# Kernel tuning notes

Measured on AMD Instinct MI355X. Metric: run time of the kernel, lower is better.

Reference implementation:

```python
import jax, jax.numpy as jnp
import numpy as np

B, T, C = 4, 2048, 1024
H = 16
D = C // H  # 64


def setup_inputs() -> dict:
    key = jax.random.key(0)
    ks = jax.random.split(key, 3)
    scale = 1.0 / np.sqrt(C)
    return {
        "x": jax.random.normal(ks[0], (B, T, C), dtype=jnp.float32),
        "W_attn": jax.random.normal(ks[1], (C, 3 * C), dtype=jnp.float32) * scale,
        "b_attn": jnp.zeros((3 * C,), dtype=jnp.float32),
        "W_proj": jax.random.normal(ks[2], (C, C), dtype=jnp.float32) * scale,
        "b_proj": jnp.zeros((C,), dtype=jnp.float32),
    }


def reference(x, W_attn, b_attn, W_proj, b_proj):
    b, t, c = x.shape
    qkv = x @ W_attn + b_attn                      # [B,T,3C]
    q, k, v = jnp.split(qkv, 3, axis=-1)           # each [B,T,C]
    to_heads = lambda z: z.reshape(b, t, H, D).transpose(0, 2, 1, 3)  # [B,H,T,D]
    q, k, v = to_heads(q), to_heads(k), to_heads(v)
    scores = jnp.einsum("bhtd,bhsd->bhts", q, k) / jnp.sqrt(jnp.float32(D))
    causal = jnp.tril(jnp.ones((t, t), dtype=bool))  # [T,T]
    scores = jnp.where(causal[None, None], scores, jnp.finfo(scores.dtype).min)
    attn = jax.nn.softmax(scores, axis=-1)           # [B,H,T,T]
    out = jnp.einsum("bhts,bhsd->bhtd", attn, v)     # [B,H,T,D]
    out = out.transpose(0, 2, 1, 3).reshape(b, t, c)
    return out @ W_proj + b_proj
```

## Files before the change

kernel.cpp:

```cpp
#include <hip/hip_runtime.h>
#include <hip/hip_bf16.h>

typedef __bf16 bf16_t;
typedef __attribute__((ext_vector_type(8))) __bf16 bf16x8;
typedef __attribute__((ext_vector_type(4))) float f32x4;
typedef __attribute__((ext_vector_type(4))) unsigned short u16x4;

#define B_DIM 4
#define T_DIM 2048
#define C_DIM 1024
#define H_DIM 16
#define D_DIM 64
#define M_TOK (B_DIM * T_DIM)
#define N_QKV (3 * C_DIM)
#define NT    (T_DIM / 64)
#define KSTR  72
#define CSC   0.18033688011112042f

__device__ __forceinline__ void gload_lds16(const bf16_t* g, bf16_t* l) {
  __builtin_amdgcn_global_load_lds((const __attribute__((address_space(1))) void*)(g),
                                   (__attribute__((address_space(3))) void*)(l), 16, 0, 0);
}

#define CVT_BLOCKS 8192
#define TRA_BLOCKS 3072
#define TRP_BLOCKS 1024
__global__ void preprocess(const float* __restrict__ x, bf16_t* __restrict__ xb,
                           const float* __restrict__ W_attn, bf16_t* __restrict__ Wat,
                           const float* __restrict__ W_proj, bf16_t* __restrict__ Wpt) {
  __shared__ float tile[32][33];
  const int bid = blockIdx.x;
  const int tid = threadIdx.x;
  if (bid < CVT_BLOCKS) {
    int i = bid * 256 + tid;
    float4 v = ((const float4*)x)[i];
    struct alignas(8) bv4 { bf16_t a, b, c, d; };
    bv4 o = {(bf16_t)v.x, (bf16_t)v.y, (bf16_t)v.z, (bf16_t)v.w};
    ((bv4*)xb)[i] = o;
    return;
  }
  const float* in; bf16_t* outp; int N, local;
  if (bid < CVT_BLOCKS + TRA_BLOCKS) {
    local = bid - CVT_BLOCKS; in = W_attn; outp = Wat; N = N_QKV;
  } else {
    local = bid - CVT_BLOCKS - TRA_BLOCKS; in = W_proj; outp = Wpt; N = C_DIM;
  }
  const int K = C_DIM;
  const int nbx = N / 32;
  const int bx = (local % nbx) * 32, by = (local / nbx) * 32;
  const int tx = tid & 31, ty = tid >> 5;
#pragma unroll
  for (int i = 0; i < 32; i += 8)
    tile[ty + i][tx] = in[(size_t)(by + ty + i) * N + bx + tx];
  __syncthreads();
#pragma unroll
  for (int i = 0; i < 32; i += 8)
    outp[(size_t)(bx + ty + i) * K + by + tx] = (bf16_t)tile[tx][ty + i];
}

#define BM 128
#define BN 128
#define BKG 64

template <typename OutT>
__global__ __launch_bounds__(256, 4)
void gemm_bt_bias(const bf16_t* __restrict__ A, const bf16_t* __restrict__ Bt,
                  const float* __restrict__ bias, OutT* __restrict__ C,
                  int M, int N, int K) {
  __shared__ alignas(16) bf16_t As[BM * BKG];
  __shared__ alignas(16) bf16_t Bs[BN * BKG];
  const int tid = threadIdx.x;
  const int lane = tid & 63;
  const int wave = tid >> 6;
  const int wr = (wave >> 1) * 64, wc = (wave & 1) * 64;
  const int quad = lane >> 4, l16 = lane & 15;
  const int row0 = blockIdx.x * BM, col0 = blockIdx.y * BN;

  const int srow = wave * 8 + (lane >> 3);
  const int scol = ((lane & 7) ^ (lane >> 3)) * 8;
  const bf16_t* Ag = A + (size_t)(row0 + srow) * K + scol;
  const bf16_t* Bg = Bt + (size_t)(col0 + srow) * K + scol;

  f32x4 acc[4][4];
#pragma unroll
  for (int i = 0; i < 4; ++i)
#pragma unroll
    for (int j = 0; j < 4; ++j)
      acc[i][j] = (f32x4){0.f, 0.f, 0.f, 0.f};

  for (int k0 = 0; k0 < K; k0 += BKG) {
    __syncthreads();
#pragma unroll
    for (int c = 0; c < 4; ++c)
      gload_lds16(Ag + k0 + (size_t)(c * 32) * K, &As[(c * 32 + wave * 8) * BKG]);
#pragma unroll
    for (int c = 0; c < 4; ++c)
      gload_lds16(Bg + k0 + (size_t)(c * 32) * K, &Bs[(c * 32 + wave * 8) * BKG]);
    __syncthreads();
#pragma unroll
    for (int kk = 0; kk < 2; ++kk) {
      const int sl = (kk * 4 + quad) ^ (l16 & 7);
      bf16x8 af[4], bfr[4];
#pragma unroll
      for (int i = 0; i < 4; ++i)
        af[i] = *(const bf16x8*)&As[(wr + i * 16 + l16) * BKG + sl * 8];
#pragma unroll
      for (int j = 0; j < 4; ++j)
        bfr[j] = *(const bf16x8*)&Bs[(wc + j * 16 + l16) * BKG + sl * 8];
#pragma unroll
      for (int i = 0; i < 4; ++i)
#pragma unroll
        for (int j = 0; j < 4; ++j)
          acc[i][j] = __builtin_amdgcn_mfma_f32_16x16x32_bf16(af[i], bfr[j], acc[i][j], 0, 0, 0);
    }
  }

#pragma unroll
  for (int i = 0; i < 4; ++i)
#pragma unroll
    for (int j = 0; j < 4; ++j) {
      int col = col0 + wc + j * 16 + l16;
      float bv = bias[col];
#pragma unroll
      for (int r = 0; r < 4; ++r) {
        int row = row0 + wr + i * 16 + quad * 4 + r;
        C[(size_t)row * N + col] = (OutT)(acc[i][j][r] + bv);
      }
    }
}

__device__ __forceinline__ float exp_row_sum(f32x4 sv[4], bool diag, bf16_t* PsW,
                                             int l16, int quad, int wave) {
  if (diag) {
    const int qr = wave * 16 + l16;
#pragma unroll
    for (int ct = 0; ct < 4; ++ct)
#pragma unroll
      for (int r = 0; r < 4; ++r)
        if (ct * 16 + quad * 4 + r > qr) sv[ct][r] = -INFINITY;
  }
  float rsum = 0.f;
#pragma unroll
  for (int ct = 0; ct < 4; ++ct) {
    u16x4 pk;
#pragma unroll
    for (int r = 0; r < 4; ++r) {
      float p = __builtin_amdgcn_exp2f(sv[ct][r] * CSC);
      rsum += p;
      pk[r] = __builtin_bit_cast(unsigned short, (bf16_t)p);
    }
    *(u16x4*)&PsW[l16 * KSTR + ct * 16 + quad * 4] = pk;
  }
  rsum += __shfl_xor(rsum, 16);
  rsum += __shfl_xor(rsum, 32);
  return rsum;
}

__global__ __launch_bounds__(256, 4)
void attn_fwd(const bf16_t* __restrict__ qkv, bf16_t* __restrict__ out) {
  __shared__ alignas(16) bf16_t Ks[64 * KSTR];
  __shared__ alignas(16) bf16_t Vt[64 * KSTR];
  __shared__ alignas(16) bf16_t Ps[4 * 16 * KSTR];

  const int tid = threadIdx.x;
  const int lane = tid & 63;
  const int wave = tid >> 6;
  const int quad = lane >> 4, l16 = lane & 15;
  const int qlo = blockIdx.x;
  const int qhi = NT - 1 - qlo;
  const int h = blockIdx.y, b = blockIdx.z;
  const size_t tokBase = (size_t)b * T_DIM;

  const bf16_t* qpl = qkv + (tokBase + qlo * 64 + wave * 16 + l16) * N_QKV + h * D_DIM;
  const bf16_t* qph = qkv + (tokBase + qhi * 64 + wave * 16 + l16) * N_QKV + h * D_DIM;
  bf16x8 ql0 = *(const bf16x8*)(qpl + quad * 8);
  bf16x8 ql1 = *(const bf16x8*)(qpl + 32 + quad * 8);
  bf16x8 qh0 = *(const bf16x8*)(qph + quad * 8);
  bf16x8 qh1 = *(const bf16x8*)(qph + 32 + quad * 8);

  f32x4 ol[4], oh[4];
#pragma unroll
  for (int dt = 0; dt < 4; ++dt) {
    ol[dt] = (f32x4){0.f, 0.f, 0.f, 0.f};
    oh[dt] = (f32x4){0.f, 0.f, 0.f, 0.f};
  }
  float ll = 0.f, lh = 0.f;

  const int tx = tid & 15, ty = tid >> 4;
  const int vswz = ((tx >> 2) & 3) * 8;
  bf16_t* PsW = &Ps[wave * 16 * KSTR];
  const f32x4 zero4 = (f32x4){0.f, 0.f, 0.f, 0.f};

  u16x4 kreg[4], vreg[4];
  const bf16_t* kb0 = qkv + (tokBase + ty * 4) * N_QKV + h * D_DIM + C_DIM + tx * 4;
#pragma unroll
  for (int r = 0; r < 4; ++r) kreg[r] = *(const u16x4*)(kb0 + (size_t)r * N_QKV);
#pragma unroll
  for (int r = 0; r < 4; ++r) vreg[r] = *(const u16x4*)(kb0 + (size_t)r * N_QKV + C_DIM);

  for (int t = 0; t <= qhi; ++t) {
    const bool lo = (t <= qlo);
    __syncthreads();
#pragma unroll
    for (int r = 0; r < 4; ++r)
      *(u16x4*)&Ks[(ty * 4 + r) * KSTR + tx * 4] = kreg[r];
#pragma unroll
    for (int i = 0; i < 4; ++i) {
      u16x4 p = (u16x4){vreg[0][i], vreg[1][i], vreg[2][i], vreg[3][i]};
      *(u16x4*)&Vt[(tx * 4 + i) * KSTR + ((ty * 4) ^ vswz)] = p;
    }
    __syncthreads();
    if (t < qhi) {
      const bf16_t* kb = qkv + (tokBase + (t + 1) * 64 + ty * 4) * N_QKV + h * D_DIM + C_DIM + tx * 4;
#pragma unroll
      for (int r = 0; r < 4; ++r) kreg[r] = *(const u16x4*)(kb + (size_t)r * N_QKV);
#pragma unroll
      for (int r = 0; r < 4; ++r) vreg[r] = *(const u16x4*)(kb + (size_t)r * N_QKV + C_DIM);
    }

    f32x4 svl[4], svh[4];
#pragma unroll
    for (int ct = 0; ct < 4; ++ct) {
      bf16x8 kf0 = *(const bf16x8*)&Ks[(ct * 16 + l16) * KSTR + quad * 8];
      bf16x8 kf1 = *(const bf16x8*)&Ks[(ct * 16 + l16) * KSTR + 32 + quad * 8];
      if (lo) {
        svl[ct] = __builtin_amdgcn_mfma_f32_16x16x32_bf16(kf0, ql0, zero4, 0, 0, 0);
        svl[ct] = __builtin_amdgcn_mfma_f32_16x16x32_bf16(kf1, ql1, svl[ct], 0, 0, 0);
      }
      svh[ct] = __builtin_amdgcn_mfma_f32_16x16x32_bf16(kf0, qh0, zero4, 0, 0, 0);
      svh[ct] = __builtin_amdgcn_mfma_f32_16x16x32_bf16(kf1, qh1, svh[ct], 0, 0, 0);
    }

    bf16x8 pl0, pl1, ph0, ph1;
    if (lo) {
      ll += exp_row_sum(svl, t == qlo, PsW, l16, quad, wave);
      pl0 = *(const bf16x8*)&PsW[l16 * KSTR + quad * 8];
      pl1 = *(const bf16x8*)&PsW[l16 * KSTR + 32 + quad * 8];
    }
    lh += exp_row_sum(svh, t == qhi, PsW, l16, quad, wave);
    ph0 = *(const bf16x8*)&PsW[l16 * KSTR + quad * 8];
    ph1 = *(const bf16x8*)&PsW[l16 * KSTR + 32 + quad * 8];

#pragma unroll
    for (int dt = 0; dt < 4; ++dt) {
      const int vcol = (quad * 8) ^ ((dt & 3) * 8);
      bf16x8 vf0 = *(const bf16x8*)&Vt[(dt * 16 + l16) * KSTR + vcol];
      bf16x8 vf1 = *(const bf16x8*)&Vt[(dt * 16 + l16) * KSTR + 32 + vcol];
      if (lo) {
        ol[dt] = __builtin_amdgcn_mfma_f32_16x16x32_bf16(vf0, pl0, ol[dt], 0, 0, 0);
        ol[dt] = __builtin_amdgcn_mfma_f32_16x16x32_bf16(vf1, pl1, ol[dt], 0, 0, 0);
      }
      oh[dt] = __builtin_amdgcn_mfma_f32_16x16x32_bf16(vf0, ph0, oh[dt], 0, 0, 0);
      oh[dt] = __builtin_amdgcn_mfma_f32_16x16x32_bf16(vf1, ph1, oh[dt], 0, 0, 0);
    }
  }

  struct alignas(8) bh4 { bf16_t a, b, c, d; };
  {
    float rl = 1.0f / ll;
    bf16_t* op = out + (tokBase + qlo * 64 + wave * 16 + l16) * C_DIM + h * D_DIM;
#pragma unroll
    for (int dt = 0; dt < 4; ++dt) {
      bh4 v = {(bf16_t)(ol[dt][0] * rl), (bf16_t)(ol[dt][1] * rl),
               (bf16_t)(ol[dt][2] * rl), (bf16_t)(ol[dt][3] * rl)};
      *(bh4*)(op + dt * 16 + quad * 4) = v;
    }
  }
  {
    float rl = 1.0f / lh;
    bf16_t* op = out + (tokBase + qhi * 64 + wave * 16 + l16) * C_DIM + h * D_DIM;
#pragma unroll
    for (int dt = 0; dt < 4; ++dt) {
      bh4 v = {(bf16_t)(oh[dt][0] * rl), (bf16_t)(oh[dt][1] * rl),
               (bf16_t)(oh[dt][2] * rl), (bf16_t)(oh[dt][3] * rl)};
      *(bh4*)(op + dt * 16 + quad * 4) = v;
    }
  }
}

extern "C" void kernel_launch(void* const* d_in, const int* in_sizes, int n_in,
                              void* d_out, int out_size, void* d_ws, size_t ws_size,
                              hipStream_t stream) {
  const float* x      = (const float*)d_in[0];
  const float* W_attn = (const float*)d_in[1];
  const float* b_attn = (const float*)d_in[2];
  const float* W_proj = (const float*)d_in[3];
  const float* b_proj = (const float*)d_in[4];
  float* out = (float*)d_out;

  char* ws = (char*)d_ws;
  bf16_t* xb   = (bf16_t*)ws;  ws += (size_t)M_TOK * C_DIM * 2;
  bf16_t* Wat  = (bf16_t*)ws;  ws += (size_t)N_QKV * C_DIM * 2;
  bf16_t* Wpt  = (bf16_t*)ws;  ws += (size_t)C_DIM * C_DIM * 2;
  bf16_t* qkv  = (bf16_t*)ws;  ws += (size_t)M_TOK * N_QKV * 2;
  bf16_t* attn = (bf16_t*)ws;  ws += (size_t)M_TOK * C_DIM * 2;

  preprocess<<<CVT_BLOCKS + TRA_BLOCKS + TRP_BLOCKS, 256, 0, stream>>>(
      x, xb, W_attn, Wat, W_proj, Wpt);

  gemm_bt_bias<bf16_t><<<dim3(M_TOK / BM, N_QKV / BN), 256, 0, stream>>>(
      xb, Wat, b_attn, qkv, M_TOK, N_QKV, C_DIM);

  attn_fwd<<<dim3(NT / 2, H_DIM, B_DIM), 256, 0, stream>>>(qkv, attn);

  gemm_bt_bias<float><<<dim3(M_TOK / BM, C_DIM / BN), 256, 0, stream>>>(
      attn, Wpt, b_proj, out, M_TOK, C_DIM, C_DIM);
}
```

Before: 256.6 us.

## Keep attention probabilities in registers and use one query tile per block

The attention kernel no longer writes exp'd probabilities to a per-wave LDS buffer and reads them back. It packs them directly into the bf16x8 MFMA operand, and the V tile is stored in LDS with a permuted column layout so the register layout matches the MFMA B operand. The paired lo/hi query-tile scheme is replaced by one query tile per block with a rotated tile index spread across heads and batches, doubling the grid and raising occupancy to 6 blocks. This removes LDS traffic and per-block register pressure, at the cost of uneven per-block work that relies on the scheduler to balance.

Measured after the change: 262.7 us. 1.02x slower.

```diff
diff --git a/kernel.cpp b/kernel.cpp
--- a/kernel.cpp
+++ b/kernel.cpp
@@ -5,6 +5,7 @@
 typedef __attribute__((ext_vector_type(8))) __bf16 bf16x8;
 typedef __attribute__((ext_vector_type(4))) float f32x4;
 typedef __attribute__((ext_vector_type(4))) unsigned short u16x4;
+typedef __attribute__((ext_vector_type(4))) unsigned int u32x4;
 
 #define B_DIM 4
 #define T_DIM 2048
@@ -129,66 +130,31 @@
     }
 }
 
-__device__ __forceinline__ float exp_row_sum(f32x4 sv[4], bool diag, bf16_t* PsW,
-                                             int l16, int quad, int wave) {
-  if (diag) {
-    const int qr = wave * 16 + l16;
-#pragma unroll
-    for (int ct = 0; ct < 4; ++ct)
-#pragma unroll
-      for (int r = 0; r < 4; ++r)
-        if (ct * 16 + quad * 4 + r > qr) sv[ct][r] = -INFINITY;
-  }
-  float rsum = 0.f;
-#pragma unroll
-  for (int ct = 0; ct < 4; ++ct) {
-    u16x4 pk;
-#pragma unroll
-    for (int r = 0; r < 4; ++r) {
-      float p = __builtin_amdgcn_exp2f(sv[ct][r] * CSC);
-      rsum += p;
-      pk[r] = __builtin_bit_cast(unsigned short, (bf16_t)p);
-    }
-    *(u16x4*)&PsW[l16 * KSTR + ct * 16 + quad * 4] = pk;
-  }
-  rsum += __shfl_xor(rsum, 16);
-  rsum += __shfl_xor(rsum, 32);
-  return rsum;
-}
-
-__global__ __launch_bounds__(256, 4)
+__global__ __launch_bounds__(256, 6)
 void attn_fwd(const bf16_t* __restrict__ qkv, bf16_t* __restrict__ out) {
   __shared__ alignas(16) bf16_t Ks[64 * KSTR];
   __shared__ alignas(16) bf16_t Vt[64 * KSTR];
-  __shared__ alignas(16) bf16_t Ps[4 * 16 * KSTR];
 
   const int tid = threadIdx.x;
   const int lane = tid & 63;
   const int wave = tid >> 6;
   const int quad = lane >> 4, l16 = lane & 15;
-  const int qlo = blockIdx.x;
-  const int qhi = NT - 1 - qlo;
   const int h = blockIdx.y, b = blockIdx.z;
+  const int q = (int)((blockIdx.x + h + 2 * b) & 31);
   const size_t tokBase = (size_t)b * T_DIM;
 
-  const bf16_t* qpl = qkv + (tokBase + qlo * 64 + wave * 16 + l16) * N_QKV + h * D_DIM;
-  const bf16_t* qph = qkv + (tokBase + qhi * 64 + wave * 16 + l16) * N_QKV + h * D_DIM;
-  bf16x8 ql0 = *(const bf16x8*)(qpl + quad * 8);
-  bf16x8 ql1 = *(const bf16x8*)(qpl + 32 + quad * 8);
-  bf16x8 qh0 = *(const bf16x8*)(qph + quad * 8);
-  bf16x8 qh1 = *(const bf16x8*)(qph + 32 + quad * 8);
-
-  f32x4 ol[4], oh[4];
-#pragma unroll
-  for (int dt = 0; dt < 4; ++dt) {
-    ol[dt] = (f32x4){0.f, 0.f, 0.f, 0.f};
-    oh[dt] = (f32x4){0.f, 0.f, 0.f, 0.f};
-  }
-  float ll = 0.f, lh = 0.f;
+  const bf16_t* qp = qkv + (tokBase + q * 64 + wave * 16 + l16) * N_QKV + h * D_DIM;
+  bf16x8 q0 = *(const bf16x8*)(qp + quad * 8);
+  bf16x8 q1 = *(const bf16x8*)(qp + 32 + quad * 8);
+
+  f32x4 o[4];
+#pragma unroll
+  for (int dt = 0; dt < 4; ++dt) o[dt] = (f32x4){0.f, 0.f, 0.f, 0.f};
+  float lsum = 0.f;
 
   const int tx = tid & 15, ty = tid >> 4;
   const int vswz = ((tx >> 2) & 3) * 8;
-  bf16_t* PsW = &Ps[wave * 16 * KSTR];
+  const int vcol = (8 * (ty & 3) + 4 * ((ty >> 2) & 1) + 32 * (ty >> 3)) ^ vswz;
   const f32x4 zero4 = (f32x4){0.f, 0.f, 0.f, 0.f};
 
   u16x4 kreg[4], vreg[4];
@@ -198,8 +164,7 @@
 #pragma unroll
   for (int r = 0; r < 4; ++r) vreg[r] = *(const u16x4*)(kb0 + (size_t)r * N_QKV + C_DIM);
 
-  for (int t = 0; t <= qhi; ++t) {
-    const bool lo = (t <= qlo);
+  for (int t = 0; t <= q; ++t) {
     __syncthreads();
 #pragma unroll
     for (int r = 0; r < 4; ++r)
@@ -207,10 +172,10 @@
 #pragma unroll
     for (int i = 0; i < 4; ++i) {
       u16x4 p = (u16x4){vreg[0][i], vreg[1][i], vreg[2][i], vreg[3][i]};
-      *(u16x4*)&Vt[(tx * 4 + i) * KSTR + ((ty * 4) ^ vswz)] = p;
-    }
-    __syncthreads();
-    if (t < qhi) {
+      *(u16x4*)&Vt[(tx * 4 + i) * KSTR + vcol] = p;
+    }
+    __syncthreads();
+    if (t < q) {
       const bf16_t* kb = qkv + (tokBase + (t + 1) * 64 + ty * 4) * N_QKV + h * D_DIM + C_DIM + tx * 4;
 #pragma unroll
       for (int r = 0; r < 4; ++r) kreg[r] = *(const u16x4*)(kb + (size_t)r * N_QKV);
@@ -218,61 +183,65 @@
       for (int r = 0; r < 4; ++r) vreg[r] = *(const u16x4*)(kb + (size_t)r * N_QKV + C_DIM);
     }
 
-    f32x4 svl[4], svh[4];
+    f32x4 sv[4];
 #pragma unroll
     for (int ct = 0; ct < 4; ++ct) {
       bf16x8 kf0 = *(const bf16x8*)&Ks[(ct * 16 + l16) * KSTR + quad * 8];
       bf16x8 kf1 = *(const bf16x8*)&Ks[(ct * 16 + l16) * KSTR + 32 + quad * 8];
-      if (lo) {
-        svl[ct] = __builtin_amdgcn_mfma_f32_16x16x32_bf16(kf0, ql0, zero4, 0, 0, 0);
-        svl[ct] = __builtin_amdgcn_mfma_f32_16x16x32_bf16(kf1, ql1, svl[ct], 0, 0, 0);
-      }
-      svh[ct] = __builtin_amdgcn_mfma_f32_16x16x32_bf16(kf0, qh0, zero4, 0, 0, 0);
-      svh[ct] = __builtin_amdgcn_mfma_f32_16x16x32_bf16(kf1, qh1, svh[ct], 0, 0, 0);
-    }
-
-    bf16x8 pl0, pl1, ph0, ph1;
-    if (lo) {
-      ll += exp_row_sum(svl, t == qlo, PsW, l16, quad, wave);
-      pl0 = *(const bf16x8*)&PsW[l16 * KSTR + quad * 8];
-      pl1 = *(const bf16x8*)&PsW[l16 * KSTR + 32 + quad * 8];
-    }
-    lh += exp_row_sum(svh, t == qhi, PsW, l16, quad, wave);
-    ph0 = *(const bf16x8*)&PsW[l16 * KSTR + quad * 8];
-    ph1 = *(const bf16x8*)&PsW[l16 * KSTR + 32 + quad * 8];
+      sv[ct] = __builtin_amdgcn_mfma_f32_16x16x32_bf16(kf0, q0, zero4, 0, 0, 0);
+      sv[ct] = __builtin_amdgcn_mfma_f32_16x16x32_bf16(kf1, q1, sv[ct], 0, 0, 0);
+    }
+    if (t == q) {
+      const int qr = wave * 16 + l16;
+#pragma unroll
+      for (int ct = 0; ct < 4; ++ct)
+#pragma unroll
+        for (int r = 0; r < 4; ++r)
+          if (ct * 16 + quad * 4 + r > qr) sv[ct][r] = -INFINITY;
+    }
+
+    float rsum = 0.f;
+    unsigned int lw[8];
+    struct alignas(4) bpair { bf16_t lo, hi; };
+#pragma unroll
+    for (int ct = 0; ct < 4; ++ct) {
+      float e0 = __builtin_amdgcn_exp2f(sv[ct][0] * CSC);
+      float e1 = __builtin_amdgcn_exp2f(sv[ct][1] * CSC);
+      float e2 = __builtin_amdgcn_exp2f(sv[ct][2] * CSC);
+      float e3 = __builtin_amdgcn_exp2f(sv[ct][3] * CSC);
+      rsum += (e0 + e1) + (e2 + e3);
+      bpair w0 = {(bf16_t)e0, (bf16_t)e1};
+      bpair w1 = {(bf16_t)e2, (bf16_t)e3};
+      lw[ct * 2 + 0] = __builtin_bit_cast(unsigned int, w0);
+      lw[ct * 2 + 1] = __builtin_bit_cast(unsigned int, w1);
+    }
+    rsum += __shfl_xor(rsum, 16);
+    rsum += __shfl_xor(rsum, 32);
+    lsum += rsum;
+
+    u32x4 pw0 = (u32x4){lw[0], lw[1], lw[2], lw[3]};
+    u32x4 pw1 = (u32x4){lw[4], lw[5], lw[6], lw[7]};
+    bf16x8 p0 = __builtin_bit_cast(bf16x8, pw0);
+    bf16x8 p1 = __builtin_bit_cast(bf16x8, pw1);
 
 #pragma unroll
     for (int dt = 0; dt < 4; ++dt) {
-      const int vcol = (quad * 8) ^ ((dt & 3) * 8);
-      bf16x8 vf0 = *(const bf16x8*)&Vt[(dt * 16 + l16) * KSTR + vcol];
-      bf16x8 vf1 = *(const bf16x8*)&Vt[(dt * 16 + l16) * KSTR + 32 + vcol];
-      if (lo) {
-        ol[dt] = __builtin_amdgcn_mfma_f32_16x16x32_bf16(vf0, pl0, ol[dt], 0, 0, 0);
-        ol[dt] = __builtin_amdgcn_mfma_f32_16x16x32_bf16(vf1, pl1, ol[dt], 0, 0, 0);
-      }
-      oh[dt] = __builtin_amdgcn_mfma_f32_16x16x32_bf16(vf0, ph0, oh[dt], 0, 0, 0);
-      oh[dt] = __builtin_amdgcn_mfma_f32_16x16x32_bf16(vf1, ph1, oh[dt], 0, 0, 0);
+      const int vc = (quad * 8) ^ (dt * 8);
+      bf16x8 vf0 = *(const bf16x8*)&Vt[(dt * 16 + l16) * KSTR + vc];
+      bf16x8 vf1 = *(const bf16x8*)&Vt[(dt * 16 + l16) * KSTR + 32 + vc];
+      o[dt] = __builtin_amdgcn_mfma_f32_16x16x32_bf16(vf0, p0, o[dt], 0, 0, 0);
+      o[dt] = __builtin_amdgcn_mfma_f32_16x16x32_bf16(vf1, p1, o[dt], 0, 0, 0);
     }
   }
 
   struct alignas(8) bh4 { bf16_t a, b, c, d; };
   {
-    float rl = 1.0f / ll;
-    bf16_t* op = out + (tokBase + qlo * 64 + wave * 16 + l16) * C_DIM + h * D_DIM;
+    float rl = 1.0f / lsum;
+    bf16_t* op = out + (tokBase + q * 64 + wave * 16 + l16) * C_DIM + h * D_DIM;
 #pragma unroll
     for (int dt = 0; dt < 4; ++dt) {
-      bh4 v = {(bf16_t)(ol[dt][0] * rl), (bf16_t)(ol[dt][1] * rl),
-               (bf16_t)(ol[dt][2] * rl), (bf16_t)(ol[dt][3] * rl)};
-      *(bh4*)(op + dt * 16 + quad * 4) = v;
-    }
-  }
-  {
-    float rl = 1.0f / lh;
-    bf16_t* op = out + (tokBase + qhi * 64 + wave * 16 + l16) * C_DIM + h * D_DIM;
-#pragma unroll
-    for (int dt = 0; dt < 4; ++dt) {
-      bh4 v = {(bf16_t)(oh[dt][0] * rl), (bf16_t)(oh[dt][1] * rl),
-               (bf16_t)(oh[dt][2] * rl), (bf16_t)(oh[dt][3] * rl)};
+      bh4 v = {(bf16_t)(o[dt][0] * rl), (bf16_t)(o[dt][1] * rl),
+               (bf16_t)(o[dt][2] * rl), (bf16_t)(o[dt][3] * rl)};
       *(bh4*)(op + dt * 16 + quad * 4) = v;
     }
   }
@@ -301,7 +270,7 @@
   gemm_bt_bias<bf16_t><<<dim3(M_TOK / BM, N_QKV / BN), 256, 0, stream>>>(
       xb, Wat, b_attn, qkv, M_TOK, N_QKV, C_DIM);
 
-  attn_fwd<<<dim3(NT / 2, H_DIM, B_DIM), 256, 0, stream>>>(qkv, attn);
+  attn_fwd<<<dim3(NT, H_DIM, B_DIM), 256, 0, stream>>>(qkv, attn);
 
   gemm_bt_bias<float><<<dim3(M_TOK / BM, C_DIM / BN), 256, 0, stream>>>(
       attn, Wpt, b_proj, out, M_TOK, C_DIM, C_DIM);
```
